# Optimization experiments

Hardware: AMD Instinct MI355X
Metric: run time of the kernel (lower is better)

## Reference

```python
import jax, jax.numpy as jnp
import numpy as np

B_BATCH, SEQ, D_MODEL, D_STATE = 8, 4096, 1024, 64
EPS = 1e-6


def setup_inputs() -> dict:
    key = jax.random.key(0)
    k = jax.random.split(key, 5)
    return {
        # inputs are clamped to [0,1] downstream, so uniform fill is natural
        "x": jax.random.uniform(k[0], (B_BATCH, SEQ, D_MODEL), jnp.float32),
        # torch.rand init for A
        "A_raw": jax.random.uniform(k[1], (D_MODEL, D_STATE), jnp.float32),
        # TopologicalLinear raw weights (sigmoid applied in forward)
        "B_w": jax.random.normal(k[2], (D_STATE, D_MODEL), jnp.float32) * 0.02,
        "C_w": jax.random.normal(k[3], (D_MODEL, D_STATE), jnp.float32) * 0.02,
        # TopologicalNorm learned per-feature gate (sigmoid(0)=0.5)
        "gamma": jnp.zeros((D_MODEL,), jnp.float32),
    }


def reference(x, A_raw, B_w, C_w, gamma):
    # x: [B, S, D]
    A = jax.nn.sigmoid(A_raw)    # [D, N] state decay gates in (0,1)
    Bm = jax.nn.sigmoid(B_w)     # [N, D] input projection (topological: sigmoid weights)
    Cm = jax.nn.sigmoid(C_w)     # [D, N] output mixing weights
    g = jax.nn.sigmoid(gamma)    # [D]   TopologicalNorm gate

    h0 = jnp.zeros((x.shape[0], A.shape[0], A.shape[1]), x.dtype)  # [B, D, N]

    def step(h, x_t):  # x_t: [B, D]
        u = x_t @ Bm.T                                        # [B, N]
        inp = u[:, None, :] * x_t[:, :, None]                 # outer(x_t, B(x_t)) -> [B, D, N]
        h = jnp.clip(h * A[None] + inp, 0.0, 1.0)             # clamped state update
        y = jnp.einsum('bdn,dn->bd', h, Cm)                   # [B, D]
        # TopologicalNorm: L1-normalize to keep values in [0,1], gated per-feature
        y = g * y / (jnp.sum(y, axis=-1, keepdims=True) + EPS)
        return h, y

    h_final, ys = jax.lax.scan(step, h0, jnp.swapaxes(x, 0, 1))  # ys: [S, B, D]
    y_final = jnp.swapaxes(ys, 0, 1)                             # [B, S, D]
    return jnp.clip(y_final + x, 0.0, 1.0), h_final
```

## Files before the change

kernel.cpp:

```cpp
#include <hip/hip_runtime.h>

#define B_BATCH 8
#define SEQ 4096
#define D_MODEL 1024
#define D_STATE 64
#define EPS 1e-6f

#define T_CHUNK 512
#define WARM 64
#define ROUND 32

__device__ __forceinline__ float sigmoidf(float v) {
    return 1.0f / (1.0f + __expf(-v));
}

__global__ __launch_bounds__(256) void prep_kernel(
    const float* __restrict__ A_raw, const float* __restrict__ B_w,
    const float* __restrict__ C_w, const float* __restrict__ gamma,
    float* __restrict__ As, float* __restrict__ Bt, float* __restrict__ Cs,
    float* __restrict__ gs) {
    int i = blockIdx.x * 256 + threadIdx.x;
    int d = i >> 6;
    int n = i & 63;
    As[i] = sigmoidf(A_raw[i]);
    Cs[i] = sigmoidf(C_w[i]);
    Bt[i] = sigmoidf(B_w[n * D_MODEL + d]);
    if (n == 0) gs[d] = sigmoidf(gamma[d]);
}

__device__ __forceinline__ void fma4(float av, const float4 bv, float* acc) {
    acc[0] = fmaf(av, bv.x, acc[0]);
    acc[1] = fmaf(av, bv.y, acc[1]);
    acc[2] = fmaf(av, bv.z, acc[2]);
    acc[3] = fmaf(av, bv.w, acc[3]);
}

__global__ __launch_bounds__(256) void u_gemm_kernel(
    const float* __restrict__ x, const float* __restrict__ Bt,
    float* __restrict__ U) {
    __shared__ float xs[64 * 68];
    __shared__ float Bs[64 * 64];
    const int tid = threadIdx.x;
    const int row0 = blockIdx.x * 64;
    const int tr = tid >> 4;
    const int tc = tid & 15;
    float acc[4][4] = {};

    for (int d0 = 0; d0 < D_MODEL; d0 += 64) {
#pragma unroll
        for (int i = 0; i < 4; ++i) {
            int f4 = i * 1024 + tid * 4;
            int r = f4 >> 6, c = f4 & 63;
            float4 v = *(const float4*)&x[(size_t)(row0 + r) * D_MODEL + d0 + c];
            *(float4*)&xs[r * 68 + c] = v;
        }
#pragma unroll
        for (int i = 0; i < 4; ++i) {
            int f4 = i * 1024 + tid * 4;
            *(float4*)&Bs[f4] = *(const float4*)&Bt[d0 * 64 + f4];
        }
        __syncthreads();
#pragma unroll
        for (int dd = 0; dd < 64; dd += 4) {
            float4 b0 = *(const float4*)&Bs[(dd + 0) * 64 + tc * 4];
            float4 b1 = *(const float4*)&Bs[(dd + 1) * 64 + tc * 4];
            float4 b2 = *(const float4*)&Bs[(dd + 2) * 64 + tc * 4];
            float4 b3 = *(const float4*)&Bs[(dd + 3) * 64 + tc * 4];
#pragma unroll
            for (int i = 0; i < 4; ++i) {
                float4 a = *(const float4*)&xs[(tr * 4 + i) * 68 + dd];
                fma4(a.x, b0, acc[i]);
                fma4(a.y, b1, acc[i]);
                fma4(a.z, b2, acc[i]);
                fma4(a.w, b3, acc[i]);
            }
        }
        __syncthreads();
    }
#pragma unroll
    for (int i = 0; i < 4; ++i) {
        float4 v = make_float4(acc[i][0], acc[i][1], acc[i][2], acc[i][3]);
        *(float4*)&U[(size_t)(row0 + tr * 4 + i) * 64 + tc * 4] = v;
    }
}

__global__ __launch_bounds__(256, 8) void scan_kernel(
    const float* __restrict__ x, const float* __restrict__ U,
    const float* __restrict__ As, const float* __restrict__ Cs,
    float* __restrict__ yraw, float* __restrict__ hout) {
    __shared__ float Ulds[ROUND * 64];
    __shared__ float xlds[ROUND * 32];
    __shared__ float ylds[ROUND * 32];
    const int tid = threadIdx.x;
    const int c = blockIdx.x & 7;
    const int d0 = ((blockIdx.x >> 3) & 31) * 32;
    const int b = blockIdx.x >> 8;
    const int g = tid >> 3;
    const int l = tid & 7;
    const int d = d0 + g;

    float h[8], a[8], cc[8];
    {
        float4 a0 = *(const float4*)&As[d * 64 + l * 8];
        float4 a1 = *(const float4*)&As[d * 64 + l * 8 + 4];
        a[0] = a0.x; a[1] = a0.y; a[2] = a0.z; a[3] = a0.w;
        a[4] = a1.x; a[5] = a1.y; a[6] = a1.z; a[7] = a1.w;
        float4 c0 = *(const float4*)&Cs[d * 64 + l * 8];
        float4 c1 = *(const float4*)&Cs[d * 64 + l * 8 + 4];
        cc[0] = c0.x; cc[1] = c0.y; cc[2] = c0.z; cc[3] = c0.w;
        cc[4] = c1.x; cc[5] = c1.y; cc[6] = c1.z; cc[7] = c1.w;
    }
#pragma unroll
    for (int j = 0; j < 8; ++j) h[j] = 0.0f;

    const size_t xbase = (size_t)b * SEQ * D_MODEL;
    const size_t ubase = (size_t)b * SEQ * 64;
    const int t_main = c * T_CHUNK;
    const int t_begin = (c == 0) ? 0 : t_main - WARM;
    const int t_end = t_main + T_CHUNK;

    for (int t0 = t_begin; t0 < t_end; t0 += ROUND) {
#pragma unroll
        for (int i = 0; i < 2; ++i) {
            int f4 = i * 1024 + tid * 4;
            *(float4*)&Ulds[f4] =
                *(const float4*)&U[ubase + (size_t)t0 * 64 + f4];
        }
        {
            int f4 = tid * 4;
            int tt = f4 >> 5, dd = f4 & 31;
            *(float4*)&xlds[f4] =
                *(const float4*)&x[xbase + (size_t)(t0 + tt) * D_MODEL + d0 + dd];
        }
        __syncthreads();

        const bool emit = (t0 >= t_main);
        if (emit) {
#pragma unroll 4
            for (int tt = 0; tt < ROUND; ++tt) {
                float4 u0 = *(const float4*)&Ulds[tt * 64 + l * 8];
                float4 u1 = *(const float4*)&Ulds[tt * 64 + l * 8 + 4];
                float xt = xlds[tt * 32 + g];
                float uu[8] = {u0.x, u0.y, u0.z, u0.w, u1.x, u1.y, u1.z, u1.w};
                float y0 = 0.0f, y1 = 0.0f;
#pragma unroll
                for (int j = 0; j < 4; ++j) {
                    h[j] = __builtin_amdgcn_fmed3f(
                        fmaf(h[j], a[j], uu[j] * xt), 0.0f, 1.0f);
                    y0 = fmaf(h[j], cc[j], y0);
                }
#pragma unroll
                for (int j = 4; j < 8; ++j) {
                    h[j] = __builtin_amdgcn_fmed3f(
                        fmaf(h[j], a[j], uu[j] * xt), 0.0f, 1.0f);
                    y1 = fmaf(h[j], cc[j], y1);
                }
                float y = y0 + y1;
                y += __shfl_xor(y, 1);
                y += __shfl_xor(y, 2);
                y += __shfl_xor(y, 4);
                if (l == 0) ylds[tt * 32 + g] = y;
            }
        } else {
#pragma unroll 4
            for (int tt = 0; tt < ROUND; ++tt) {
                float4 u0 = *(const float4*)&Ulds[tt * 64 + l * 8];
                float4 u1 = *(const float4*)&Ulds[tt * 64 + l * 8 + 4];
                float xt = xlds[tt * 32 + g];
                float uu[8] = {u0.x, u0.y, u0.z, u0.w, u1.x, u1.y, u1.z, u1.w};
#pragma unroll
                for (int j = 0; j < 8; ++j) {
                    h[j] = __builtin_amdgcn_fmed3f(
                        fmaf(h[j], a[j], uu[j] * xt), 0.0f, 1.0f);
                }
            }
        }
        __syncthreads();

        if (emit) {
            int f4 = tid * 4;
            int tt = f4 >> 5, dd = f4 & 31;
            *(float4*)&yraw[xbase + (size_t)(t0 + tt) * D_MODEL + d0 + dd] =
                *(const float4*)&ylds[f4];
        }
    }

    if (c == (SEQ / T_CHUNK) - 1) {
        float4 h0 = make_float4(h[0], h[1], h[2], h[3]);
        float4 h1 = make_float4(h[4], h[5], h[6], h[7]);
        size_t hoff = ((size_t)b * D_MODEL + d) * 64 + l * 8;
        *(float4*)&hout[hoff] = h0;
        *(float4*)&hout[hoff + 4] = h1;
    }
}

__global__ __launch_bounds__(256) void norm_kernel(
    const float* __restrict__ x, const float* __restrict__ gs,
    float* __restrict__ y) {
    __shared__ float red[4];
    const int tid = threadIdx.x;
    const size_t base = (size_t)blockIdx.x * D_MODEL;

    float4 yv = *(const float4*)&y[base + tid * 4];
    float s = yv.x + yv.y + yv.z + yv.w;
#pragma unroll
    for (int off = 1; off < 64; off <<= 1) s += __shfl_xor(s, off);
    if ((tid & 63) == 0) red[tid >> 6] = s;
    __syncthreads();
    float tot = red[0] + red[1] + red[2] + red[3];
    float inv = 1.0f / (tot + EPS);

    float4 xv = *(const float4*)&x[base + tid * 4];
    float4 gv = *(const float4*)&gs[tid * 4];
    float4 o;
    o.x = __builtin_amdgcn_fmed3f(fmaf(gv.x * yv.x, inv, xv.x), 0.0f, 1.0f);
    o.y = __builtin_amdgcn_fmed3f(fmaf(gv.y * yv.y, inv, xv.y), 0.0f, 1.0f);
    o.z = __builtin_amdgcn_fmed3f(fmaf(gv.z * yv.z, inv, xv.z), 0.0f, 1.0f);
    o.w = __builtin_amdgcn_fmed3f(fmaf(gv.w * yv.w, inv, xv.w), 0.0f, 1.0f);
    *(float4*)&y[base + tid * 4] = o;
}

extern "C" void kernel_launch(void* const* d_in, const int* in_sizes, int n_in,
                              void* d_out, int out_size, void* d_ws,
                              size_t ws_size, hipStream_t stream) {
    const float* x     = (const float*)d_in[0];
    const float* A_raw = (const float*)d_in[1];
    const float* B_w   = (const float*)d_in[2];
    const float* C_w   = (const float*)d_in[3];
    const float* gamma = (const float*)d_in[4];

    float* out  = (float*)d_out;
    float* yout = out;
    float* hout = out + (size_t)B_BATCH * SEQ * D_MODEL;

    float* ws = (float*)d_ws;
    float* As = ws;
    float* Bt = ws + 65536;
    float* Cs = ws + 131072;
    float* gs = ws + 196608;
    float* U  = ws + 197632;

    prep_kernel<<<256, 256, 0, stream>>>(A_raw, B_w, C_w, gamma, As, Bt, Cs, gs);
    u_gemm_kernel<<<(B_BATCH * SEQ) / 64, 256, 0, stream>>>(x, Bt, U);
    scan_kernel<<<B_BATCH * (D_MODEL / 32) * (SEQ / T_CHUNK), 256, 0, stream>>>(
        x, U, As, Cs, yout, hout);
    norm_kernel<<<B_BATCH * SEQ, 256, 0, stream>>>(x, gs, yout);
}
```

Before: 595.3 us.

## Skip scan steps when minimum input product saturates state to one

Computes per-timestep minima of U and x tiles during the load, and when min(x)*min(U) >= 1 for a wave's features, every state entry saturates to 1 after the clamp. Such steps are skipped and y is set to the precomputed row sum of C, with the state materialised lazily as all-ones before the next real step. This removes the FMA/clamp/shuffle work for saturated steps, which are very common here because x is uniform in [0,1] and U = x·sigmoid(B)^T with 1024 terms is large. The cost is extra min-reduction shuffles and a per-step wave-uniform branch; correctness relies on h·a >= 0, which holds since h and a are non-negative.

```diff
diff --git a/kernel.cpp b/kernel.cpp
--- a/kernel.cpp
+++ b/kernel.cpp
@@ -91,6 +91,8 @@
     __shared__ float Ulds[ROUND * 64];
     __shared__ float xlds[ROUND * 32];
     __shared__ float ylds[ROUND * 32];
+    __shared__ float uminlds[ROUND];
+    __shared__ float xminlds[4 * ROUND];
     const int tid = threadIdx.x;
     const int c = blockIdx.x & 7;
     const int d0 = ((blockIdx.x >> 3) & 31) * 32;
@@ -98,6 +100,7 @@
     const int g = tid >> 3;
     const int l = tid & 7;
     const int d = d0 + g;
+    const int w = tid >> 6;
 
     float h[8], a[8], cc[8];
     {
@@ -110,8 +113,14 @@
         cc[0] = c0.x; cc[1] = c0.y; cc[2] = c0.z; cc[3] = c0.w;
         cc[4] = c1.x; cc[5] = c1.y; cc[6] = c1.z; cc[7] = c1.w;
     }
+    float crow = ((cc[0] + cc[1]) + (cc[2] + cc[3])) +
+                 ((cc[4] + cc[5]) + (cc[6] + cc[7]));
+    crow += __shfl_xor(crow, 1);
+    crow += __shfl_xor(crow, 2);
+    crow += __shfl_xor(crow, 4);
 #pragma unroll
     for (int j = 0; j < 8; ++j) h[j] = 0.0f;
+    bool hone = false;
 
     const size_t xbase = (size_t)b * SEQ * D_MODEL;
     const size_t ubase = (size_t)b * SEQ * 64;
@@ -120,58 +129,113 @@
     const int t_end = t_main + T_CHUNK;
 
     for (int t0 = t_begin; t0 < t_end; t0 += ROUND) {
-#pragma unroll
-        for (int i = 0; i < 2; ++i) {
-            int f4 = i * 1024 + tid * 4;
-            *(float4*)&Ulds[f4] =
-                *(const float4*)&U[ubase + (size_t)t0 * 64 + f4];
+        {
+            const float* Up = &U[ubase + (size_t)t0 * 64];
+            float4 v0 = *(const float4*)&Up[tid * 4];
+            float4 v1 = *(const float4*)&Up[1024 + tid * 4];
+            *(float4*)&Ulds[tid * 4] = v0;
+            *(float4*)&Ulds[1024 + tid * 4] = v1;
+            float m0 = fminf(fminf(v0.x, v0.y), fminf(v0.z, v0.w));
+            float m1 = fminf(fminf(v1.x, v1.y), fminf(v1.z, v1.w));
+#pragma unroll
+            for (int s = 1; s < 16; s <<= 1) {
+                m0 = fminf(m0, __shfl_xor(m0, s));
+                m1 = fminf(m1, __shfl_xor(m1, s));
+            }
+            if ((tid & 15) == 0) {
+                uminlds[tid >> 4] = m0;
+                uminlds[(tid >> 4) + 16] = m1;
+            }
         }
         {
             int f4 = tid * 4;
             int tt = f4 >> 5, dd = f4 & 31;
-            *(float4*)&xlds[f4] =
+            float4 v =
                 *(const float4*)&x[xbase + (size_t)(t0 + tt) * D_MODEL + d0 + dd];
+            *(float4*)&xlds[f4] = v;
+            float m = fminf(fminf(v.x, v.y), fminf(v.z, v.w));
+            m = fminf(m, __shfl_xor(m, 1));
+            if ((tid & 1) == 0) xminlds[((tid >> 1) & 3) * ROUND + tt] = m;
         }
         __syncthreads();
 
         const bool emit = (t0 >= t_main);
         if (emit) {
-#pragma unroll 4
-            for (int tt = 0; tt < ROUND; ++tt) {
-                float4 u0 = *(const float4*)&Ulds[tt * 64 + l * 8];
-                float4 u1 = *(const float4*)&Ulds[tt * 64 + l * 8 + 4];
-                float xt = xlds[tt * 32 + g];
-                float uu[8] = {u0.x, u0.y, u0.z, u0.w, u1.x, u1.y, u1.z, u1.w};
-                float y0 = 0.0f, y1 = 0.0f;
-#pragma unroll
-                for (int j = 0; j < 4; ++j) {
-                    h[j] = __builtin_amdgcn_fmed3f(
-                        fmaf(h[j], a[j], uu[j] * xt), 0.0f, 1.0f);
-                    y0 = fmaf(h[j], cc[j], y0);
+            for (int tq = 0; tq < ROUND; tq += 4) {
+                float4 um4 = *(const float4*)&uminlds[tq];
+                float4 xm4 = *(const float4*)&xminlds[w * ROUND + tq];
+                float umv[4] = {um4.x, um4.y, um4.z, um4.w};
+                float xmv[4] = {xm4.x, xm4.y, xm4.z, xm4.w};
+#pragma unroll
+                for (int k = 0; k < 4; ++k) {
+                    const int tt = tq + k;
+                    float p = xmv[k] * umv[k];
+                    if (__builtin_amdgcn_readfirstlane(__float_as_int(p)) >=
+                        0x3f800000) {
+                        hone = true;
+                        if (l == 0) ylds[tt * 32 + g] = crow;
+                    } else {
+                        if (hone) {
+#pragma unroll
+                            for (int j = 0; j < 8; ++j) h[j] = 1.0f;
+                            hone = false;
+                        }
+                        float xt = xlds[tt * 32 + g];
+                        float4 u0 = *(const float4*)&Ulds[tt * 64 + l * 8];
+                        float4 u1 = *(const float4*)&Ulds[tt * 64 + l * 8 + 4];
+                        float uu[8] = {u0.x, u0.y, u0.z, u0.w,
+                                       u1.x, u1.y, u1.z, u1.w};
+                        float y0 = 0.0f, y1 = 0.0f;
+#pragma unroll
+                        for (int j = 0; j < 4; ++j) {
+                            h[j] = __builtin_amdgcn_fmed3f(
+                                fmaf(h[j], a[j], uu[j] * xt), 0.0f, 1.0f);
+                            y0 = fmaf(h[j], cc[j], y0);
+                        }
+#pragma unroll
+                        for (int j = 4; j < 8; ++j) {
+                            h[j] = __builtin_amdgcn_fmed3f(
+                                fmaf(h[j], a[j], uu[j] * xt), 0.0f, 1.0f);
+                            y1 = fmaf(h[j], cc[j], y1);
+                        }
+                        float y = y0 + y1;
+                        y += __shfl_xor(y, 1);
+                        y += __shfl_xor(y, 2);
+                        y += __shfl_xor(y, 4);
+                        if (l == 0) ylds[tt * 32 + g] = y;
+                    }
                 }
-#pragma unroll
-                for (int j = 4; j < 8; ++j) {
-                    h[j] = __builtin_amdgcn_fmed3f(
-                        fmaf(h[j], a[j], uu[j] * xt), 0.0f, 1.0f);
-                    y1 = fmaf(h[j], cc[j], y1);
-                }
-                float y = y0 + y1;
-                y += __shfl_xor(y, 1);
-                y += __shfl_xor(y, 2);
-                y += __shfl_xor(y, 4);
-                if (l == 0) ylds[tt * 32 + g] = y;
             }
         } else {
-#pragma unroll 4
-            for (int tt = 0; tt < ROUND; ++tt) {
-                float4 u0 = *(const float4*)&Ulds[tt * 64 + l * 8];
-                float4 u1 = *(const float4*)&Ulds[tt * 64 + l * 8 + 4];
-                float xt = xlds[tt * 32 + g];
-                float uu[8] = {u0.x, u0.y, u0.z, u0.w, u1.x, u1.y, u1.z, u1.w};
-#pragma unroll
-                for (int j = 0; j < 8; ++j) {
-                    h[j] = __builtin_amdgcn_fmed3f(
-                        fmaf(h[j], a[j], uu[j] * xt), 0.0f, 1.0f);
+            for (int tq = 0; tq < ROUND; tq += 4) {
+                float4 um4 = *(const float4*)&uminlds[tq];
+                float4 xm4 = *(const float4*)&xminlds[w * ROUND + tq];
+                float umv[4] = {um4.x, um4.y, um4.z, um4.w};
+                float xmv[4] = {xm4.x, xm4.y, xm4.z, xm4.w};
+#pragma unroll
+                for (int k = 0; k < 4; ++k) {
+                    const int tt = tq + k;
+                    float p = xmv[k] * umv[k];
+                    if (__builtin_amdgcn_readfirstlane(__float_as_int(p)) >=
+                        0x3f800000) {
+                        hone = true;
+                    } else {
+                        if (hone) {
+#pragma unroll
+                            for (int j = 0; j < 8; ++j) h[j] = 1.0f;
+                            hone = false;
+                        }
+                        float xt = xlds[tt * 32 + g];
+                        float4 u0 = *(const float4*)&Ulds[tt * 64 + l * 8];
+                        float4 u1 = *(const float4*)&Ulds[tt * 64 + l * 8 + 4];
+                        float uu[8] = {u0.x, u0.y, u0.z, u0.w,
+                                       u1.x, u1.y, u1.z, u1.w};
+#pragma unroll
+                        for (int j = 0; j < 8; ++j) {
+                            h[j] = __builtin_amdgcn_fmed3f(
+                                fmaf(h[j], a[j], uu[j] * xt), 0.0f, 1.0f);
+                        }
+                    }
                 }
             }
         }
@@ -186,6 +250,10 @@
     }
 
     if (c == (SEQ / T_CHUNK) - 1) {
+        if (hone) {
+#pragma unroll
+            for (int j = 0; j < 8; ++j) h[j] = 1.0f;
+        }
         float4 h0 = make_float4(h[0], h[1], h[2], h[3]);
         float4 h1 = make_float4(h[4], h[5], h[6], h[7]);
         size_t hoff = ((size_t)b * D_MODEL + d) * 64 + l * 8;
```

New measurement: 722.8 us. 1.21x slower.
